# Optimization experiments

Hardware: AMD Instinct MI355X
Metric: run time of the kernel (lower is better)

The kernel has to match this reference:

```python
import jax, jax.numpy as jnp
import numpy as np

B, S, F, H, D = 32, 512, 32, 8, 300   # batch, seq, n_features, hidden_dim, n_dim_model
FH = min(D, F)                        # flattened GRN hidden = min(n_dim_model, n_features)


def _p(key, shape, scale=0.05):
    return (jax.random.normal(key, shape) * scale).astype(jnp.float32)


def setup_inputs() -> dict:
    key = jax.random.key(0)
    ks = jax.random.split(key, 16)
    return {
        "x": jax.random.normal(ks[0], (B, S, F), dtype=jnp.float32),
        "pre_w": _p(ks[1], (F, H)), "pre_b": _p(ks[2], (F, H)),
        "sg_fc1_w": _p(ks[3], (F, H, H)), "sg_fc1_b": _p(ks[4], (F, H)),
        "sg_fc2_w": _p(ks[5], (F, H, D)), "sg_fc2_b": _p(ks[6], (F, D)),
        "sg_gate_w": _p(ks[7], (F, D, 2 * D)), "sg_gate_b": _p(ks[8], (F, 2 * D)),
        "sg_ln_g": jnp.ones((F, D), jnp.float32), "sg_ln_b": jnp.zeros((F, D), jnp.float32),
        "fl_fc1_w": _p(ks[9], (F * H, FH)), "fl_fc1_b": _p(ks[10], (FH,)),
        "fl_fc2_w": _p(ks[11], (FH, F)), "fl_fc2_b": _p(ks[12], (F,)),
        "fl_gate_w": _p(ks[13], (F, 2 * F)), "fl_gate_b": _p(ks[14], (2 * F,)),
        "fl_ln_g": jnp.ones((F,), jnp.float32), "fl_ln_b": jnp.zeros((F,), jnp.float32),
    }


def _interp_last(x, out_dim):
    # torch F.interpolate(mode='linear', align_corners=True) along the last axis
    in_dim = x.shape[-1]
    pos = jnp.arange(out_dim) * ((in_dim - 1) / (out_dim - 1))
    lo = jnp.floor(pos).astype(jnp.int32)
    hi = jnp.minimum(lo + 1, in_dim - 1)
    w = (pos - lo.astype(pos.dtype)).astype(x.dtype)
    return x[..., lo] * (1 - w) + x[..., hi] * w


def _layer_norm(x, g, b, eps=1e-5):
    m = jnp.mean(x, axis=-1, keepdims=True)
    v = jnp.var(x, axis=-1, keepdims=True)
    return (x - m) * jax.lax.rsqrt(v + eps) * g + b


def _forward(x, pre_w, pre_b, sg_fc1_w, sg_fc1_b, sg_fc2_w, sg_fc2_b,
             sg_gate_w, sg_gate_b, sg_ln_g, sg_ln_b,
             fl_fc1_w, fl_fc1_b, fl_fc2_w, fl_fc2_b, fl_gate_w, fl_gate_b,
             fl_ln_g, fl_ln_b):
    # per-feature prescaler: Linear(1, H) for each of F features, batched
    pre = x[..., None] * pre_w + pre_b                                   # [B,S,F,H]

    # per-feature GRN (H -> H -> D), batched over the feature axis f
    h = jax.nn.elu(jnp.einsum('bsfh,fhk->bsfk', pre, sg_fc1_w) + sg_fc1_b)
    h = jnp.einsum('bsfk,fkd->bsfd', h, sg_fc2_w) + sg_fc2_b             # [B,S,F,D]
    g = jnp.einsum('bsfd,fdp->bsfp', h, sg_gate_w) + sg_gate_b           # [B,S,F,2D]
    glu = g[..., :D] * jax.nn.sigmoid(g[..., D:])
    residual = _interp_last(pre, D)                                      # H -> D interpolate projection
    outputs = _layer_norm(glu + residual, sg_ln_g, sg_ln_b)              # [B,S,F,D]

    # flattened GRN on concatenated prescaler outputs (F*H -> FH -> F)
    flat = pre.reshape(pre.shape[0], pre.shape[1], F * H)                # matches torch.cat order
    fh = jax.nn.elu(flat @ fl_fc1_w + fl_fc1_b)
    fh = fh @ fl_fc2_w + fl_fc2_b                                        # [B,S,F]
    fg = fh @ fl_gate_w + fl_gate_b                                      # [B,S,2F]
    fglu = fg[..., :F] * jax.nn.sigmoid(fg[..., F:])
    wlogits = _layer_norm(fglu + _interp_last(flat, F), fl_ln_g, fl_ln_b)
    w = jax.nn.softmax(wlogits, axis=-1)                                 # [B,S,F]

    out = jnp.einsum('bsfd,bsf->bsd', outputs, w)                        # softmax-weighted sum over features
    return out, w[..., None, :]                                          # weights unsqueezed at dim -2


def reference(x, pre_w, pre_b, sg_fc1_w, sg_fc1_b, sg_fc2_w, sg_fc2_b,
              sg_gate_w, sg_gate_b, sg_ln_g, sg_ln_b,
              fl_fc1_w, fl_fc1_b, fl_fc2_w, fl_fc2_b, fl_gate_w, fl_gate_b,
              fl_ln_g, fl_ln_b):
    return _forward(x, pre_w, pre_b, sg_fc1_w, sg_fc1_b, sg_fc2_w, sg_fc2_b,
                    sg_gate_w, sg_gate_b, sg_ln_g, sg_ln_b,
                    fl_fc1_w, fl_fc1_b, fl_fc2_w, fl_fc2_b, fl_gate_w, fl_gate_b,
                    fl_ln_g, fl_ln_b)
```

## Files before the change

kernel.cpp:

```cpp
#include <hip/hip_runtime.h>
#include <hip/hip_bf16.h>

#define NB 32
#define NS 512
#define NF 32
#define NH 8
#define ND 300
#define NTOK (NB*NS)
#define TPW 8
#define WPB 4
#define TPB (TPW*WPB)

using bf16 = __hip_bfloat16;
typedef float v2f __attribute__((ext_vector_type(2)));

__device__ __forceinline__ float rcpf_(float x){ return __builtin_amdgcn_rcpf(x); }
__device__ __forceinline__ float rsqf_(float x){ return __builtin_amdgcn_rsqf(x); }
__device__ __forceinline__ float sigm(float x){ return rcpf_(1.0f + __expf(-x)); }
__device__ __forceinline__ float eluf(float x){ return x > 0.0f ? x : __expf(x) - 1.0f; }

__device__ __forceinline__ v2f fma2(v2f a, v2f b, v2f c){
    return __builtin_elementwise_fma(a, b, c);
}
__device__ __forceinline__ v2f fma2s(float s, v2f b, v2f c){
    return __builtin_elementwise_fma((v2f){s, s}, b, c);
}

template<int BF16>
__device__ __forceinline__ float ldf(const void* p, size_t i){
    if (BF16) return __bfloat162float(((const bf16*)p)[i]);
    return ((const float*)p)[i];
}
template<int BF16>
__device__ __forceinline__ void stf(void* p, size_t i, float v){
    if (BF16) ((bf16*)p)[i] = __float2bfloat16(v);
    else      ((float*)p)[i] = v;
}

__device__ __forceinline__ bool is_bf16(const void* ones){
    return *(const unsigned*)ones == 0x3F803F80u;
}

__device__ __forceinline__ v2f unpk(unsigned u){
    return (v2f){ __int_as_float((int)(u << 16)),
                  __int_as_float((int)(u & 0xFFFF0000u)) };
}
__device__ __forceinline__ unsigned pack_bf(float a, float b){
    bf16 ha = __float2bfloat16(a), hb = __float2bfloat16(b);
    return (unsigned)*(unsigned short*)&ha | ((unsigned)*(unsigned short*)&hb << 16);
}

template<int CTRL>
__device__ __forceinline__ float dppadd(float v){
    return v + __int_as_float(__builtin_amdgcn_update_dpp(
        0, __float_as_int(v), CTRL, 0xF, 0xF, true));
}
template<int CTRL>
__device__ __forceinline__ float dppmax(float v){
    return fmaxf(v, __int_as_float(__builtin_amdgcn_update_dpp(
        __float_as_int(v), __float_as_int(v), CTRL, 0xF, 0xF, false)));
}
__device__ __forceinline__ float rlane(float v, int l){
    return __int_as_float(__builtin_amdgcn_readlane(__float_as_int(v), l));
}
__device__ __forceinline__ float wsum64(float v){
    v = dppadd<0x111>(v); v = dppadd<0x112>(v); v = dppadd<0x114>(v); v = dppadd<0x118>(v);
    v = dppadd<0x142>(v); v = dppadd<0x143>(v);
    return rlane(v, 63);
}
__device__ __forceinline__ float rsum32(float v){
    v = dppadd<0x111>(v); v = dppadd<0x112>(v); v = dppadd<0x114>(v); v = dppadd<0x118>(v);
    return rlane(v, 15) + rlane(v, 31);
}
__device__ __forceinline__ float rmax32(float v){
    v = dppmax<0x111>(v); v = dppmax<0x112>(v); v = dppmax<0x114>(v); v = dppmax<0x118>(v);
    return fmaxf(rlane(v, 15), rlane(v, 31));
}

template<int BF16>
__device__ void precompute_body(const void* __restrict__ W2, const void* __restrict__ b2,
                                const void* __restrict__ Wg, const void* __restrict__ bg,
                                const void* __restrict__ sg_g, const void* __restrict__ sg_b,
                                unsigned* __restrict__ Crow,
                                float (*part)[16][18], float* w2s, float* b2s)
{
    const int tid = threadIdx.x;
    const int l = tid & 15;
    const int q = tid >> 4;
    const int fd = blockIdx.x * 16 + l;
    const int f = fd / 300;
    const int d = fd % 300;

    const int fLo = (blockIdx.x * 16) / 300;
    const int fHi = (blockIdx.x * 16 + 15) / 300;

    for (int ff = 0; ff <= fHi - fLo; ++ff) {
        for (int idx = tid; idx < 2400; idx += 256)
            w2s[ff * 2400 + idx] = ldf<BF16>(W2, (size_t)(fLo + ff) * 2400 + idx);
        for (int idx = tid; idx < 300; idx += 256)
            b2s[ff * 300 + idx] = ldf<BF16>(b2, (size_t)(fLo + ff) * 300 + idx);
    }
    __syncthreads();

    const float* myW2 = w2s + (f - fLo) * 2400;
    const float* myB2 = b2s + (f - fLo) * 300;
    const size_t WgA = (size_t)f * 180000 + d;

    const int m0 = q * 19;
    const int m1 = (m0 + 19 < 300) ? m0 + 19 : 300;
    float accA[8] = {0,0,0,0,0,0,0,0};
    float accB[8] = {0,0,0,0,0,0,0,0};
    float bA = 0.f, bB = 0.f;
    for (int m = m0; m < m1; ++m) {
        float wa = ldf<BF16>(Wg, WgA + (size_t)m * 600);
        float wb = ldf<BF16>(Wg, WgA + (size_t)m * 600 + 300);
        #pragma unroll
        for (int k = 0; k < 8; ++k) {
            float w2v = myW2[k * 300 + m];
            accA[k] += w2v * wa;
            accB[k] += w2v * wb;
        }
        bA += myB2[m] * wa;
        bB += myB2[m] * wb;
    }
    #pragma unroll
    for (int k = 0; k < 8; ++k) { part[q][l][k] = accA[k]; part[q][l][8 + k] = accB[k]; }
    part[q][l][16] = bA;
    part[q][l][17] = bB;
    __syncthreads();

    if (tid < 192) {
        const int pl_ = tid / 12, v = tid % 12;
        const int fd2 = blockIdx.x * 16 + pl_;
        const int f2 = fd2 / 300, d2 = fd2 % 300;
        unsigned* row = Crow + (size_t)fd2 * 12;
        if (v < 8) {
            float sA = 0.f, sB = 0.f;
            #pragma unroll
            for (int qq = 0; qq < 16; ++qq) { sA += part[qq][pl_][v]; sB += part[qq][pl_][8 + v]; }
            row[v] = pack_bf(sA, sB);
        } else if (v == 8) {
            float s = 0.f;
            #pragma unroll
            for (int qq = 0; qq < 16; ++qq) s += part[qq][pl_][16];
            row[8] = __float_as_uint(s + ldf<BF16>(bg, (size_t)f2 * 600 + d2));
        } else if (v == 9) {
            float s = 0.f;
            #pragma unroll
            for (int qq = 0; qq < 16; ++qq) s += part[qq][pl_][17];
            row[9] = __float_as_uint(s + ldf<BF16>(bg, (size_t)f2 * 600 + d2 + 300));
        } else if (v == 10) {
            row[10] = __float_as_uint(ldf<BF16>(sg_g, (size_t)f2 * 300 + d2));
        } else {
            row[11] = __float_as_uint(ldf<BF16>(sg_b, (size_t)f2 * 300 + d2));
        }
    }
}

__global__ void precompute_kernel(const void* __restrict__ W2, const void* __restrict__ b2,
                                  const void* __restrict__ Wg, const void* __restrict__ bg,
                                  const void* __restrict__ sg_g, const void* __restrict__ sg_b,
                                  unsigned* __restrict__ Crow)
{
    __shared__ float part[16][16][18];
    __shared__ float w2s[2 * 2400];
    __shared__ float b2s[2 * 300];
    if (is_bf16(sg_g))
        precompute_body<1>(W2, b2, Wg, bg, sg_g, sg_b, Crow, part, w2s, b2s);
    else
        precompute_body<0>(W2, b2, Wg, bg, sg_g, sg_b, Crow, part, w2s, b2s);
}

template<int BF16>
__device__ void vsn_body(const void* __restrict__ x,
                         const void* __restrict__ pre_w, const void* __restrict__ pre_b,
                         const void* __restrict__ W1,    const void* __restrict__ b1,
                         const void* __restrict__ fl1w,  const void* __restrict__ fl1b,
                         const void* __restrict__ fl2w,  const void* __restrict__ fl2b,
                         const void* __restrict__ flgw,  const void* __restrict__ flgb,
                         const void* __restrict__ flng,  const void* __restrict__ flnb,
                         const unsigned* __restrict__ Crow,
                         void* __restrict__ d_out, float* preS_, unsigned* hS_)
{
    void* outMain = d_out;
    void* outW    = (char*)d_out + (size_t)NTOK * ND * (BF16 ? 2 : 4);

    const int tid  = threadIdx.x;
    const int wave = tid >> 6;
    const int lane = tid & 63;
    const int tokBase = blockIdx.x * TPB + wave * TPW;

    float*    myPre = preS_ + wave * (TPW * 256);
    unsigned* myH   = hS_   + wave * (TPW * 128);

    {
        float pw[4], pb[4];
        #pragma unroll
        for (int q = 0; q < 4; ++q) {
            pw[q] = ldf<BF16>(pre_w, 4 * lane + q);
            pb[q] = ldf<BF16>(pre_b, 4 * lane + q);
        }
        const int fidx = lane >> 1;
        #pragma unroll
        for (int t = 0; t < TPW; ++t) {
            float xv = ldf<BF16>(x, (size_t)(tokBase + t) * NF + fidx);
            float4 v;
            v.x = xv * pw[0] + pb[0];
            v.y = xv * pw[1] + pb[1];
            v.z = xv * pw[2] + pb[2];
            v.w = xv * pw[3] + pb[3];
            *(float4*)(&myPre[t * 256 + 4 * lane]) = v;
        }
    }

    {
        const int f  = lane >> 1;
        const int kh = (lane & 1) * 4;
        float w1r[8][4], b1r[4];
        #pragma unroll
        for (int m = 0; m < 8; ++m)
            #pragma unroll
            for (int q = 0; q < 4; ++q)
                w1r[m][q] = ldf<BF16>(W1, (size_t)(f * 8 + m) * 8 + kh + q);
        #pragma unroll
        for (int q = 0; q < 4; ++q) b1r[q] = ldf<BF16>(b1, f * 8 + kh + q);

        #pragma unroll
        for (int t = 0; t < TPW; ++t) {
            float pr[8];
            float4 pA = *(const float4*)(&myPre[t * 256 + f * 8]);
            float4 pB = *(const float4*)(&myPre[t * 256 + f * 8 + 4]);
            pr[0]=pA.x; pr[1]=pA.y; pr[2]=pA.z; pr[3]=pA.w;
            pr[4]=pB.x; pr[5]=pB.y; pr[6]=pB.z; pr[7]=pB.w;
            float a[4] = {b1r[0], b1r[1], b1r[2], b1r[3]};
            #pragma unroll
            for (int m = 0; m < 8; ++m)
                #pragma unroll
                for (int q = 0; q < 4; ++q)
                    a[q] += pr[m] * w1r[m][q];
            uint2 hp;
            hp.x = pack_bf(eluf(a[0]), eluf(a[1]));
            hp.y = pack_bf(eluf(a[2]), eluf(a[3]));
            *(uint2*)(&myH[t * 128 + 2 * lane]) = hp;
        }
    }

    const int jj = lane & 31;
    const int hB = lane >> 5;
    float wreg[TPW];
    {
        float f1b = (hB == 0) ? ldf<BF16>(fl1b, jj) : 0.0f;
        v2f p1v[4];
        #pragma unroll
        for (int g = 0; g < 4; ++g) p1v[g] = (v2f){f1b, f1b};
        for (int kg = 0; kg < 32; ++kg) {
            const int kk = hB * 128 + kg * 4;
            float4 pr[TPW];
            #pragma unroll
            for (int t = 0; t < TPW; ++t)
                pr[t] = *(const float4*)(&myPre[t * 256 + kk]);
            float w0 = ldf<BF16>(fl1w, (size_t)(kk + 0) * 32 + jj);
            float w1 = ldf<BF16>(fl1w, (size_t)(kk + 1) * 32 + jj);
            float w2 = ldf<BF16>(fl1w, (size_t)(kk + 2) * 32 + jj);
            float w3 = ldf<BF16>(fl1w, (size_t)(kk + 3) * 32 + jj);
            #pragma unroll
            for (int g = 0; g < 4; ++g) {
                p1v[g] = fma2((v2f){pr[2*g].x, pr[2*g+1].x}, (v2f){w0, w0}, p1v[g]);
                p1v[g] = fma2((v2f){pr[2*g].y, pr[2*g+1].y}, (v2f){w1, w1}, p1v[g]);
                p1v[g] = fma2((v2f){pr[2*g].z, pr[2*g+1].z}, (v2f){w2, w2}, p1v[g]);
                p1v[g] = fma2((v2f){pr[2*g].w, pr[2*g+1].w}, (v2f){w3, w3}, p1v[g]);
            }
        }
        float fhv[TPW];
        #pragma unroll
        for (int t = 0; t < TPW; ++t) {
            float p1 = (t & 1) ? p1v[t >> 1].y : p1v[t >> 1].x;
            fhv[t] = eluf(p1 + __shfl_xor(p1, 32));
        }

        float p2[TPW];
        float f2b = ldf<BF16>(fl2b, jj);
        #pragma unroll
        for (int t = 0; t < TPW; ++t) p2[t] = f2b;
        #pragma unroll
        for (int k = 0; k < 32; ++k) {
            float wv = ldf<BF16>(fl2w, k * 32 + jj);
            #pragma unroll
            for (int t = 0; t < TPW; ++t) p2[t] += rlane(fhv[t], k) * wv;
        }
        float p3[TPW];
        float fgbv = ldf<BF16>(flgb, lane);
        #pragma unroll
        for (int t = 0; t < TPW; ++t) p3[t] = fgbv;
        #pragma unroll
        for (int k = 0; k < 32; ++k) {
            float wv = ldf<BF16>(flgw, k * 64 + lane);
            #pragma unroll
            for (int t = 0; t < TPW; ++t) p3[t] += rlane(p2[t], k) * wv;
        }

        float lng = ldf<BF16>(flng, jj), lnb = ldf<BF16>(flnb, jj);
        float posB = (float)jj * (255.0f / 31.0f);
        int loB = (int)floorf(posB); loB = loB < 0 ? 0 : (loB > 254 ? 254 : loB);
        float frB = posB - (float)loB;

        #pragma unroll
        for (int t = 0; t < TPW; ++t) {
            float fgA  = __shfl(p3[t], jj);
            float fgB  = __shfl(p3[t], jj + 32);
            float fglu = fgA * sigm(fgB);
            float pl = myPre[t * 256 + loB];
            float ph = myPre[t * 256 + loB + 1];
            float tv = fglu + pl + frB * (ph - pl);
            float S1 = rsum32(tv);
            float S2 = rsum32(tv * tv);
            float mean = S1 * (1.0f / 32.0f);
            float var  = fmaxf(S2 * (1.0f / 32.0f) - mean * mean, 0.0f);
            float rs   = rsqf_(var + 1e-5f);
            float wl   = (tv - mean) * rs * lng + lnb;
            float mx   = rmax32(wl);
            float e    = __expf(wl - mx);
            float ss   = rsum32(e);
            float wv   = e * rcpf_(ss);
            wreg[t] = wv;
            if (lane < 32) stf<BF16>(outW, (size_t)(tokBase + t) * NF + lane, wv);
        }
    }

    int lo_[5]; float fr_[5];
    #pragma unroll
    for (int i = 0; i < 5; ++i) {
        int d = i * 64 + lane;
        float pos = (float)d * (7.0f / 299.0f);
        int lo = (int)floorf(pos); lo = lo < 0 ? 0 : (lo > 6 ? 6 : lo);
        lo_[i] = lo; fr_[i] = pos - (float)lo;
    }

    float acc[TPW][5];
    #pragma unroll
    for (int t = 0; t < TPW; ++t)
        #pragma unroll
        for (int i = 0; i < 5; ++i) acc[t][i] = 0.0f;

    for (int f = 0; f < NF; ++f) {
        v2f  P[5][8];
        float bcA[5], bcB[5], lgv[5], lbv[5];
        #pragma unroll
        for (int i = 0; i < 5; ++i) {
            int d = i * 64 + lane;
            bool ok = (d < ND);
            const uint4* row = (const uint4*)(Crow + ((size_t)f * ND + (ok ? d : ND - 1)) * 12);
            uint4 c0 = row[0], c1 = row[1], c2 = row[2];
            P[i][0] = unpk(c0.x); P[i][1] = unpk(c0.y);
            P[i][2] = unpk(c0.z); P[i][3] = unpk(c0.w);
            P[i][4] = unpk(c1.x); P[i][5] = unpk(c1.y);
            P[i][6] = unpk(c1.z); P[i][7] = unpk(c1.w);
            bcA[i] = __uint_as_float(c2.x);
            bcB[i] = __uint_as_float(c2.y);
            lgv[i] = __uint_as_float(c2.z);
            lbv[i] = __uint_as_float(c2.w);
        }

        #pragma unroll
        for (int t = 0; t < TPW; ++t) {
            uint4 hp = *(const uint4*)(&myH[t * 128 + f * 4]);
            v2f h01 = unpk(hp.x), h23 = unpk(hp.y), h45 = unpk(hp.z), h67 = unpk(hp.w);

            float tt[5], a1 = 0.f, a2 = 0.f;
            #pragma unroll
            for (int i = 0; i < 5; ++i) {
                int d = i * 64 + lane;
                bool ok = (d < ND);
                v2f g = {bcA[i], bcB[i]};
                g = fma2s(h01.x, P[i][0], g);
                g = fma2s(h01.y, P[i][1], g);
                g = fma2s(h23.x, P[i][2], g);
                g = fma2s(h23.y, P[i][3], g);
                g = fma2s(h45.x, P[i][4], g);
                g = fma2s(h45.y, P[i][5], g);
                g = fma2s(h67.x, P[i][6], g);
                g = fma2s(h67.y, P[i][7], g);
                int base = f * 8 + lo_[i];
                float pl = myPre[t * 256 + base];
                float ph = myPre[t * 256 + base + 1];
                float tv = g.x * sigm(g.y) + pl + fr_[i] * (ph - pl);
                tv = ok ? tv : 0.0f;
                tt[i] = tv; a1 += tv; a2 += tv * tv;
            }

            float S1 = wsum64(a1);
            float S2 = wsum64(a2);
            float mean = S1 * (1.0f / 300.0f);
            float var  = fmaxf(S2 * (1.0f / 300.0f) - mean * mean, 0.0f);
            float rs   = rsqf_(var + 1e-5f);
            float wf   = rlane(wreg[t], f);
            float c1v  = wf * rs;
            float c2v  = -c1v * mean;
            #pragma unroll
            for (int i = 0; i < 5; ++i) {
                int d = i * 64 + lane;
                if (d < ND) {
                    float v = fmaf(c1v, tt[i], c2v);
                    acc[t][i] = fmaf(lgv[i], v, fmaf(wf, lbv[i], acc[t][i]));
                }
            }
        }
    }

    #pragma unroll
    for (int t = 0; t < TPW; ++t) {
        const size_t tok = (size_t)tokBase + t;
        #pragma unroll
        for (int i = 0; i < 5; ++i) {
            int d = i * 64 + lane;
            if (d < ND) stf<BF16>(outMain, tok * ND + d, acc[t][i]);
        }
    }
}

__launch_bounds__(256)
__global__ void vsn_main(const void* __restrict__ x,
                         const void* __restrict__ pre_w, const void* __restrict__ pre_b,
                         const void* __restrict__ W1,    const void* __restrict__ b1,
                         const void* __restrict__ fl1w,  const void* __restrict__ fl1b,
                         const void* __restrict__ fl2w,  const void* __restrict__ fl2b,
                         const void* __restrict__ flgw,  const void* __restrict__ flgb,
                         const void* __restrict__ flng,  const void* __restrict__ flnb,
                         const unsigned* __restrict__ Crow, void* __restrict__ d_out)
{
    __shared__ float    preS_[WPB * TPW * 256];
    __shared__ unsigned hS_[WPB * TPW * 128];
    if (is_bf16(flng))
        vsn_body<1>(x, pre_w, pre_b, W1, b1, fl1w, fl1b, fl2w, fl2b,
                    flgw, flgb, flng, flnb, Crow, d_out, preS_, hS_);
    else
        vsn_body<0>(x, pre_w, pre_b, W1, b1, fl1w, fl1b, fl2w, fl2b,
                    flgw, flgb, flng, flnb, Crow, d_out, preS_, hS_);
}

extern "C" void kernel_launch(void* const* d_in, const int* in_sizes, int n_in,
                              void* d_out, int out_size, void* d_ws, size_t ws_size,
                              hipStream_t stream)
{
    const void* x     = d_in[0];
    const void* pre_w = d_in[1];
    const void* pre_b = d_in[2];
    const void* W1    = d_in[3];
    const void* b1    = d_in[4];
    const void* W2    = d_in[5];
    const void* b2    = d_in[6];
    const void* Wg    = d_in[7];
    const void* bg    = d_in[8];
    const void* sg_g  = d_in[9];
    const void* sg_b  = d_in[10];
    const void* fl1w  = d_in[11];
    const void* fl1b  = d_in[12];
    const void* fl2w  = d_in[13];
    const void* fl2b  = d_in[14];
    const void* flgw  = d_in[15];
    const void* flgb  = d_in[16];
    const void* flng  = d_in[17];
    const void* flnb  = d_in[18];

    unsigned* Crow = (unsigned*)d_ws;

    precompute_kernel<<<600, 256, 0, stream>>>(W2, b2, Wg, bg, sg_g, sg_b, Crow);

    vsn_main<<<NTOK / TPB, 256, 0, stream>>>(x, pre_w, pre_b, W1, b1,
        fl1w, fl1b, fl2w, fl2b, flgw, flgb, flng, flnb, Crow, d_out);
}
```

Baseline: 316.3 us.

## Halve tokens per wave, restructure gate precompute, fold log2e into sigmoid

Tokens per wave drop from 8 to 4, so the main kernel launches twice as many blocks and holds fewer per-thread accumulators, which is meant to raise occupancy and parallelism. The precompute kernel is rebuilt: one block covers a (feature, 64-column chunk) pair, W2 is stored transposed in shared memory for vector reads, the reduction runs over 8 waves, and each Crow row is written with uint4 stores. The gate's sigmoid-half coefficients are pre-multiplied by log2(e) so the main kernel can call exp2 directly instead of exp. In exchange, fl1w and the other per-wave weight reads are amortised over fewer tokens.

```diff
diff --git a/kernel.cpp b/kernel.cpp
--- a/kernel.cpp
+++ b/kernel.cpp
@@ -7,9 +7,11 @@
 #define NH 8
 #define ND 300
 #define NTOK (NB*NS)
-#define TPW 8
+#define TPW 4
 #define WPB 4
 #define TPB (TPW*WPB)
+
+#define L2E 1.4426950408889634f
 
 using bf16 = __hip_bfloat16;
 typedef float v2f __attribute__((ext_vector_type(2)));
@@ -17,6 +19,7 @@
 __device__ __forceinline__ float rcpf_(float x){ return __builtin_amdgcn_rcpf(x); }
 __device__ __forceinline__ float rsqf_(float x){ return __builtin_amdgcn_rsqf(x); }
 __device__ __forceinline__ float sigm(float x){ return rcpf_(1.0f + __expf(-x)); }
+__device__ __forceinline__ float sigm2(float x){ return rcpf_(1.0f + __builtin_amdgcn_exp2f(-x)); }
 __device__ __forceinline__ float eluf(float x){ return x > 0.0f ? x : __expf(x) - 1.0f; }
 
 __device__ __forceinline__ v2f fma2(v2f a, v2f b, v2f c){
@@ -82,78 +85,81 @@
                                 const void* __restrict__ Wg, const void* __restrict__ bg,
                                 const void* __restrict__ sg_g, const void* __restrict__ sg_b,
                                 unsigned* __restrict__ Crow,
-                                float (*part)[16][18], float* w2s, float* b2s)
+                                float* __restrict__ w2t, float* __restrict__ b2s,
+                                float (*part)[64][18])
 {
-    const int tid = threadIdx.x;
-    const int l = tid & 15;
-    const int q = tid >> 4;
-    const int fd = blockIdx.x * 16 + l;
-    const int f = fd / 300;
-    const int d = fd % 300;
-
-    const int fLo = (blockIdx.x * 16) / 300;
-    const int fHi = (blockIdx.x * 16 + 15) / 300;
-
-    for (int ff = 0; ff <= fHi - fLo; ++ff) {
-        for (int idx = tid; idx < 2400; idx += 256)
-            w2s[ff * 2400 + idx] = ldf<BF16>(W2, (size_t)(fLo + ff) * 2400 + idx);
-        for (int idx = tid; idx < 300; idx += 256)
-            b2s[ff * 300 + idx] = ldf<BF16>(b2, (size_t)(fLo + ff) * 300 + idx);
-    }
+    const int tid  = threadIdx.x;
+    const int lane = tid & 63;
+    const int wv   = tid >> 6;
+    const int f    = blockIdx.x & 31;
+    const int c    = blockIdx.x >> 5;
+    const int d    = c * 64 + lane;
+    const int dc   = d < 299 ? d : 299;
+
+    for (int idx = tid; idx < 2400; idx += 512) {
+        int m = idx >> 3, k = idx & 7;
+        w2t[idx] = ldf<BF16>(W2, (size_t)f * 2400 + (size_t)k * 300 + m);
+    }
+    if (tid < 300) b2s[tid] = ldf<BF16>(b2, (size_t)f * 300 + tid);
     __syncthreads();
 
-    const float* myW2 = w2s + (f - fLo) * 2400;
-    const float* myB2 = b2s + (f - fLo) * 300;
-    const size_t WgA = (size_t)f * 180000 + d;
-
-    const int m0 = q * 19;
-    const int m1 = (m0 + 19 < 300) ? m0 + 19 : 300;
-    float accA[8] = {0,0,0,0,0,0,0,0};
-    float accB[8] = {0,0,0,0,0,0,0,0};
-    float bA = 0.f, bB = 0.f;
+    v2f aA01 = {0,0}, aA23 = {0,0}, aA45 = {0,0}, aA67 = {0,0};
+    v2f aB01 = {0,0}, aB23 = {0,0}, aB45 = {0,0}, aB67 = {0,0};
+    float bAa = 0.f, bBa = 0.f;
+
+    const int m0 = (wv * 300) >> 3;
+    const int m1 = ((wv + 1) * 300) >> 3;
+    const size_t WgF = (size_t)f * 180000 + dc;
+    #pragma unroll 4
     for (int m = m0; m < m1; ++m) {
-        float wa = ldf<BF16>(Wg, WgA + (size_t)m * 600);
-        float wb = ldf<BF16>(Wg, WgA + (size_t)m * 600 + 300);
-        #pragma unroll
-        for (int k = 0; k < 8; ++k) {
-            float w2v = myW2[k * 300 + m];
-            accA[k] += w2v * wa;
-            accB[k] += w2v * wb;
-        }
-        bA += myB2[m] * wa;
-        bB += myB2[m] * wb;
-    }
-    #pragma unroll
-    for (int k = 0; k < 8; ++k) { part[q][l][k] = accA[k]; part[q][l][8 + k] = accB[k]; }
-    part[q][l][16] = bA;
-    part[q][l][17] = bB;
+        float wa = ldf<BF16>(Wg, WgF + (size_t)m * 600);
+        float wb = ldf<BF16>(Wg, WgF + (size_t)m * 600 + 300);
+        float4 wk0 = *(const float4*)(w2t + m * 8);
+        float4 wk1 = *(const float4*)(w2t + m * 8 + 4);
+        aA01 = fma2s(wa, (v2f){wk0.x, wk0.y}, aA01);
+        aA23 = fma2s(wa, (v2f){wk0.z, wk0.w}, aA23);
+        aA45 = fma2s(wa, (v2f){wk1.x, wk1.y}, aA45);
+        aA67 = fma2s(wa, (v2f){wk1.z, wk1.w}, aA67);
+        aB01 = fma2s(wb, (v2f){wk0.x, wk0.y}, aB01);
+        aB23 = fma2s(wb, (v2f){wk0.z, wk0.w}, aB23);
+        aB45 = fma2s(wb, (v2f){wk1.x, wk1.y}, aB45);
+        aB67 = fma2s(wb, (v2f){wk1.z, wk1.w}, aB67);
+        float b2v = b2s[m];
+        bAa += b2v * wa;
+        bBa += b2v * wb;
+    }
+
+    {
+        float* p = part[wv][lane];
+        p[0]  = aA01.x; p[1]  = aA01.y; p[2]  = aA23.x; p[3]  = aA23.y;
+        p[4]  = aA45.x; p[5]  = aA45.y; p[6]  = aA67.x; p[7]  = aA67.y;
+        p[8]  = aB01.x; p[9]  = aB01.y; p[10] = aB23.x; p[11] = aB23.y;
+        p[12] = aB45.x; p[13] = aB45.y; p[14] = aB67.x; p[15] = aB67.y;
+        p[16] = bAa;    p[17] = bBa;
+    }
     __syncthreads();
 
-    if (tid < 192) {
-        const int pl_ = tid / 12, v = tid % 12;
-        const int fd2 = blockIdx.x * 16 + pl_;
-        const int f2 = fd2 / 300, d2 = fd2 % 300;
-        unsigned* row = Crow + (size_t)fd2 * 12;
-        if (v < 8) {
-            float sA = 0.f, sB = 0.f;
-            #pragma unroll
-            for (int qq = 0; qq < 16; ++qq) { sA += part[qq][pl_][v]; sB += part[qq][pl_][8 + v]; }
-            row[v] = pack_bf(sA, sB);
-        } else if (v == 8) {
-            float s = 0.f;
-            #pragma unroll
-            for (int qq = 0; qq < 16; ++qq) s += part[qq][pl_][16];
-            row[8] = __float_as_uint(s + ldf<BF16>(bg, (size_t)f2 * 600 + d2));
-        } else if (v == 9) {
-            float s = 0.f;
-            #pragma unroll
-            for (int qq = 0; qq < 16; ++qq) s += part[qq][pl_][17];
-            row[9] = __float_as_uint(s + ldf<BF16>(bg, (size_t)f2 * 600 + d2 + 300));
-        } else if (v == 10) {
-            row[10] = __float_as_uint(ldf<BF16>(sg_g, (size_t)f2 * 300 + d2));
-        } else {
-            row[11] = __float_as_uint(ldf<BF16>(sg_b, (size_t)f2 * 300 + d2));
-        }
+    if (tid < 64 && d < 300) {
+        float s[18];
+        #pragma unroll
+        for (int v = 0; v < 18; ++v) {
+            float t0 = part[0][lane][v] + part[1][lane][v];
+            float t1 = part[2][lane][v] + part[3][lane][v];
+            float t2 = part[4][lane][v] + part[5][lane][v];
+            float t3 = part[6][lane][v] + part[7][lane][v];
+            s[v] = (t0 + t1) + (t2 + t3);
+        }
+        unsigned dw[12];
+        #pragma unroll
+        for (int k = 0; k < 8; ++k) dw[k] = pack_bf(s[k], s[8 + k] * L2E);
+        dw[8]  = __float_as_uint(s[16] + ldf<BF16>(bg, (size_t)f * 600 + d));
+        dw[9]  = __float_as_uint((s[17] + ldf<BF16>(bg, (size_t)f * 600 + d + 300)) * L2E);
+        dw[10] = __float_as_uint(ldf<BF16>(sg_g, (size_t)f * 300 + d));
+        dw[11] = __float_as_uint(ldf<BF16>(sg_b, (size_t)f * 300 + d));
+        unsigned* row = Crow + (size_t)(f * 300 + d) * 12;
+        *(uint4*)(row + 0) = make_uint4(dw[0], dw[1], dw[2],  dw[3]);
+        *(uint4*)(row + 4) = make_uint4(dw[4], dw[5], dw[6],  dw[7]);
+        *(uint4*)(row + 8) = make_uint4(dw[8], dw[9], dw[10], dw[11]);
     }
 }
 
@@ -162,13 +168,13 @@
                                   const void* __restrict__ sg_g, const void* __restrict__ sg_b,
                                   unsigned* __restrict__ Crow)
 {
-    __shared__ float part[16][16][18];
-    __shared__ float w2s[2 * 2400];
-    __shared__ float b2s[2 * 300];
+    __shared__ float w2t[2400];
+    __shared__ float b2s[300];
+    __shared__ float part[8][64][18];
     if (is_bf16(sg_g))
-        precompute_body<1>(W2, b2, Wg, bg, sg_g, sg_b, Crow, part, w2s, b2s);
+        precompute_body<1>(W2, b2, Wg, bg, sg_g, sg_b, Crow, w2t, b2s, part);
     else
-        precompute_body<0>(W2, b2, Wg, bg, sg_g, sg_b, Crow, part, w2s, b2s);
+        precompute_body<0>(W2, b2, Wg, bg, sg_g, sg_b, Crow, w2t, b2s, part);
 }
 
 template<int BF16>
@@ -250,9 +256,9 @@
     float wreg[TPW];
     {
         float f1b = (hB == 0) ? ldf<BF16>(fl1b, jj) : 0.0f;
-        v2f p1v[4];
-        #pragma unroll
-        for (int g = 0; g < 4; ++g) p1v[g] = (v2f){f1b, f1b};
+        v2f p1v[TPW / 2];
+        #pragma unroll
+        for (int g = 0; g < TPW / 2; ++g) p1v[g] = (v2f){f1b, f1b};
         for (int kg = 0; kg < 32; ++kg) {
             const int kk = hB * 128 + kg * 4;
             float4 pr[TPW];
@@ -264,7 +270,7 @@
             float w2 = ldf<BF16>(fl1w, (size_t)(kk + 2) * 32 + jj);
             float w3 = ldf<BF16>(fl1w, (size_t)(kk + 3) * 32 + jj);
             #pragma unroll
-            for (int g = 0; g < 4; ++g) {
+            for (int g = 0; g < TPW / 2; ++g) {
                 p1v[g] = fma2((v2f){pr[2*g].x, pr[2*g+1].x}, (v2f){w0, w0}, p1v[g]);
                 p1v[g] = fma2((v2f){pr[2*g].y, pr[2*g+1].y}, (v2f){w1, w1}, p1v[g]);
                 p1v[g] = fma2((v2f){pr[2*g].z, pr[2*g+1].z}, (v2f){w2, w2}, p1v[g]);
@@ -383,7 +389,7 @@
                 int base = f * 8 + lo_[i];
                 float pl = myPre[t * 256 + base];
                 float ph = myPre[t * 256 + base + 1];
-                float tv = g.x * sigm(g.y) + pl + fr_[i] * (ph - pl);
+                float tv = g.x * sigm2(g.y) + pl + fr_[i] * (ph - pl);
                 tv = ok ? tv : 0.0f;
                 tt[i] = tv; a1 += tv; a2 += tv * tv;
             }
@@ -464,7 +470,7 @@
 
     unsigned* Crow = (unsigned*)d_ws;
 
-    precompute_kernel<<<600, 256, 0, stream>>>(W2, b2, Wg, bg, sg_g, sg_b, Crow);
+    precompute_kernel<<<160, 512, 0, stream>>>(W2, b2, Wg, bg, sg_g, sg_b, Crow);
 
     vsn_main<<<NTOK / TPB, 256, 0, stream>>>(x, pre_w, pre_b, W1, b1,
         fl1w, fl1b, fl2w, fl2b, flgw, flgb, flng, flnb, Crow, d_out);
```

Result: slower. 326.8 us (+3.3%).
